# Performance work log

Measured on AMD Instinct MI355X. Metric: run time of the kernel, lower is better.

The kernel has to match this reference:

```python
import math
import jax, jax.numpy as jnp
import numpy as np
from jax import lax

HEADS = 8
DIM_HEAD = 32
DIM = 256
FF_INNER = DIM * 4
EPS = 1e-5


def conv1x1(x, w, b=None):
    # x: (B,C,H,W), w: (O,C)
    y = jnp.einsum('bchw,oc->bohw', x, w)
    return y if b is None else y + b[None, :, None, None]


def dwconv3(x, w, b):
    # depthwise 3x3, padding=1; w: (C,1,3,3)
    C = x.shape[1]
    y = lax.conv_general_dilated(x, w, (1, 1), 'SAME',
                                 dimension_numbers=('NCHW', 'OIHW', 'NCHW'),
                                 feature_group_count=C)
    return y + b[None, :, None, None]


def instance_norm(x):
    m = jnp.mean(x, axis=(2, 3), keepdims=True)
    v = jnp.var(x, axis=(2, 3), keepdims=True)
    return (x - m) / jnp.sqrt(v + EPS)


def chan_layer_norm(x, g, b):
    m = jnp.mean(x, axis=1, keepdims=True)
    v = jnp.var(x, axis=1, keepdims=True)
    return (x - m) / jnp.sqrt(v + EPS) * g + b


def l2norm(t):
    # F.normalize(t, dim=-1): normalize along last (width) axis
    n = jnp.sqrt(jnp.sum(t * t, axis=-1, keepdims=True))
    return t / jnp.maximum(n, 1e-12)


def dpsa(x, g, bc, w_qkv, w_out, b_out):
    B, C, H, W = x.shape
    kH = int(math.ceil(math.sqrt(H)))
    kW = int(math.ceil(math.sqrt(W)))
    x = chan_layer_norm(x, g, bc)
    qkv = conv1x1(x, w_qkv)                       # (B, 3*inner, H, W)
    q, k, v = jnp.split(qkv, 3, axis=1)
    fold = lambda t: t.reshape(B * HEADS, DIM_HEAD, H, W)
    q, k, v = fold(q), fold(k), fold(v)
    q, k = l2norm(q), l2norm(k)
    BH = B * HEADS
    q_probe = jnp.sum(jnp.abs(q), axis=(2, 3))    # (BH, d)
    if kH < H:
        k_height = jnp.sum(jnp.abs(k), axis=3)    # (BH, d, H)
        score_r = jnp.einsum('bc,bch->bh', q_probe, k_height)
        _, idx_h = lax.top_k(score_r, kH)          # (BH, kH)
        idx = jnp.broadcast_to(idx_h[:, None, :, None], (BH, DIM_HEAD, kH, W))
        k = jnp.take_along_axis(k, idx, axis=2)
        v = jnp.take_along_axis(v, idx, axis=2)
    if kW < W:
        k_width = jnp.sum(jnp.abs(k), axis=2)     # (BH, d, W)
        score_c = jnp.einsum('bc,bcw->bw', q_probe, k_width)
        _, idx_w = lax.top_k(score_c, kW)          # (BH, kW)
        idx = jnp.broadcast_to(idx_w[:, None, None, :], (BH, DIM_HEAD, k.shape[2], kW))
        k = jnp.take_along_axis(k, idx, axis=3)
        v = jnp.take_along_axis(v, idx, axis=3)
    flat = lambda t: t.transpose(0, 2, 3, 1).reshape(BH, -1, DIM_HEAD)
    q, k, v = flat(q), flat(k), flat(v)            # (BH, HW, d), (BH, kHkW, d)
    sim = jnp.einsum('bid,bjd->bij', q, k)         # note: original never applies scale
    attn = jax.nn.softmax(sim, axis=-1)
    out = jnp.einsum('bij,bjd->bid', attn, v)
    out = out.reshape(B, HEADS, H, W, DIM_HEAD).transpose(0, 1, 4, 2, 3)
    out = out.reshape(B, HEADS * DIM_HEAD, H, W)
    return conv1x1(out, w_out, b_out)


def hpb_forward(x, g, bc, w_qkv, w_out, b_out, w_dw, b_dw, w_comb, b_comb,
                w_ff1, b_ff1, w_ffdw, b_ffdw, w_ff2, b_ff2):
    attn_branch = dpsa(x, g, bc, w_qkv, w_out, b_out)
    conv_branch = dwconv3(x, w_dw, b_dw)
    combined = jnp.concatenate([attn_branch, conv_branch], axis=1)
    attn_out = conv1x1(combined, w_comb, b_comb) + x
    # feed-forward: 1x1 conv -> IN -> GELU -> Residual(dw3x3 -> IN -> GELU) -> 1x1 conv -> IN
    h = jax.nn.gelu(instance_norm(conv1x1(attn_out, w_ff1, b_ff1)), approximate=False)
    h = h + jax.nn.gelu(instance_norm(dwconv3(h, w_ffdw, b_ffdw)), approximate=False)
    return instance_norm(conv1x1(h, w_ff2, b_ff2))


def setup_inputs() -> dict:
    key = jax.random.key(0)
    ks = jax.random.split(key, 12)
    s = 0.02
    inner = HEADS * DIM_HEAD
    return {
        'x': jax.random.normal(ks[0], (16, DIM, 64, 64), dtype=jnp.float32),
        'g': jnp.ones((1, DIM, 1, 1), jnp.float32),
        'bc': jnp.zeros((1, DIM, 1, 1), jnp.float32),
        'w_qkv': jax.random.normal(ks[1], (inner * 3, DIM), jnp.float32) * s,
        'w_out': jax.random.normal(ks[2], (DIM, inner), jnp.float32) * s,
        'b_out': jnp.zeros((DIM,), jnp.float32),
        'w_dw': jax.random.normal(ks[3], (DIM, 1, 3, 3), jnp.float32) * s,
        'b_dw': jnp.zeros((DIM,), jnp.float32),
        'w_comb': jax.random.normal(ks[4], (DIM, DIM * 2), jnp.float32) * s,
        'b_comb': jnp.zeros((DIM,), jnp.float32),
        'w_ff1': jax.random.normal(ks[5], (FF_INNER, DIM), jnp.float32) * s,
        'b_ff1': jnp.zeros((FF_INNER,), jnp.float32),
        'w_ffdw': jax.random.normal(ks[6], (FF_INNER, 1, 3, 3), jnp.float32) * s,
        'b_ffdw': jnp.zeros((FF_INNER,), jnp.float32),
        'w_ff2': jax.random.normal(ks[7], (DIM, FF_INNER), jnp.float32) * s,
        'b_ff2': jnp.zeros((DIM,), jnp.float32),
    }


def reference(x, g, bc, w_qkv, w_out, b_out, w_dw, b_dw, w_comb, b_comb,
              w_ff1, b_ff1, w_ffdw, b_ffdw, w_ff2, b_ff2):
    return hpb_forward(x, g, bc, w_qkv, w_out, b_out, w_dw, b_dw, w_comb, b_comb,
                       w_ff1, b_ff1, w_ffdw, b_ffdw, w_ff2, b_ff2)
```

## Files before the change

### kernel.cpp

```cpp
#include <hip/hip_runtime.h>
#include <math.h>

#define NB 16
#define NC 256
#define NP 4096
#define NHEADS 8
#define NDH 32
#define NBH 128
#define NFF 1024
#define CEPS 1e-5f

typedef short s16x8 __attribute__((ext_vector_type(8)));
typedef float f32x4 __attribute__((ext_vector_type(4)));

__global__ __launch_bounds__(256) void diag_fill(float* __restrict__ out, float val, int n)
{
    int i = blockIdx.x * 256 + threadIdx.x;
    if (i < n) out[i] = val;
}

__device__ inline unsigned short f2bf(float f) {
    unsigned u = __float_as_uint(f);
    return (unsigned short)((u + 0x7FFFu + ((u >> 16) & 1u)) >> 16);
}
__device__ inline float bf2f(unsigned short h) { return __uint_as_float(((unsigned)h) << 16); }
__device__ inline void split2(float f, unsigned short& hi, unsigned short& lo) {
    hi = f2bf(f);
    lo = f2bf(f - bf2f(hi));
}
__device__ inline void split_rn(float f, unsigned short& hi, unsigned short& lo) {
    unsigned u = __float_as_uint(f);
    unsigned tt = u + 0x8000u;
    hi = (unsigned short)(tt >> 16);
    float r = f - __uint_as_float(tt & 0xffff0000u);
    lo = (unsigned short)((__float_as_uint(r) + 0x8000u) >> 16);
}
__device__ inline unsigned pack_hl(float f) {
    unsigned short h, lo; split2(f, h, lo);
    return ((unsigned)h << 16) | (unsigned)lo;
}
__device__ inline float packf(float f) { return __uint_as_float(pack_hl(f)); }

__global__ __launch_bounds__(256) void pack_wg_kernel(
    const float* __restrict__ w, const float* __restrict__ g,
    unsigned* __restrict__ pw, int n)
{
    int i = blockIdx.x * 256 + threadIdx.x;
    if (i < n) pw[i] = pack_hl(w[i] * g[i & 255]);
}

__global__ __launch_bounds__(256) void cln_stats_kernel(
    const float* __restrict__ x, float* __restrict__ rs, float* __restrict__ mrs)
{
    __shared__ double red[512];
    int t = threadIdx.x;
    int i = t & 63, q = t >> 6;
    int col = blockIdx.x * 64 + i;
    int b = col >> 12, p = col & 4095;
    const float* src = x + (size_t)b * NC * NP + (size_t)(q * 64) * NP + p;
    double s = 0.0, s2 = 0.0;
    #pragma unroll 8
    for (int c = 0; c < 64; c++) { float v = src[(size_t)c * NP]; s += v; s2 += (double)v * v; }
    red[q * 64 + i] = s; red[256 + q * 64 + i] = s2;
    __syncthreads();
    if (q == 0) {
        double S  = red[i] + red[64 + i] + red[128 + i] + red[192 + i];
        double S2 = red[256 + i] + red[320 + i] + red[384 + i] + red[448 + i];
        double mean = S * (1.0 / 256.0);
        double var = S2 * (1.0 / 256.0) - mean * mean;
        double r = 1.0 / sqrt(var + (double)CEPS);
        rs[col]  = (float)r;
        mrs[col] = (float)(mean * r);
    }
}

__global__ __launch_bounds__(256) void ab_kernel(
    const float* __restrict__ wq, const float* __restrict__ g, const float* __restrict__ bc,
    float* __restrict__ Aab, float* __restrict__ Bab)
{
    int o = blockIdx.x * 256 + threadIdx.x;
    if (o >= 768) return;
    double a = 0.0, bsum = 0.0;
    for (int c = 0; c < 256; c++) {
        double w = wq[o * 256 + c];
        a += w * (double)g[c];
        bsum += w * (double)bc[c];
    }
    Aab[o] = (float)a; Bab[o] = (float)bsum;
}

__global__ __launch_bounds__(256) void fuse_comb_kernel(
    const float* __restrict__ w_comb, const float* __restrict__ w_out,
    const float* __restrict__ b_out, const float* __restrict__ b_comb,
    unsigned* __restrict__ pwF, float* __restrict__ bF)
{
    int idx = blockIdx.x * 256 + threadIdx.x;
    int o = idx >> 9, cc = idx & 511;
    float val;
    if (cc < 256) {
        double s = 0.0;
        for (int k = 0; k < 256; k++)
            s += (double)w_comb[o * 512 + k] * (double)w_out[k * 256 + cc];
        val = (float)s;
    } else {
        val = w_comb[o * 512 + cc];
    }
    pwF[idx] = pack_hl(val);
    if (idx < 256) {
        double s = 0.0;
        for (int k = 0; k < 256; k++)
            s += (double)w_comb[idx * 512 + k] * (double)b_out[k];
        bF[idx] = (float)(s + (double)b_comb[idx]);
    }
}

template<bool PACKO, bool PACKA, bool CLN, bool OBF16, bool BBF16>
__global__ __launch_bounds__(512) void gemm_mfma(
    const float* __restrict__ inA, int sA, int C1,
    const float* __restrict__ inB, int sB, int Ctot,
    const float* __restrict__ Wt, const float* __restrict__ bias,
    const float* __restrict__ resid, float* __restrict__ out, int sO, int O,
    const float* __restrict__ rs, const float* __restrict__ mrs,
    const float* __restrict__ Aab, const float* __restrict__ Bab,
    float* __restrict__ qrow, float* __restrict__ kheight)
{
    __shared__ __align__(16) unsigned short Ah[128 * 32], Al[128 * 32];
    __shared__ __align__(16) unsigned short Bh[128 * 32];
    __shared__ __align__(16) unsigned short Bl[BBF16 ? 16 : 128 * 32];
    char* cAh = (char*)Ah; char* cAl = (char*)Al;
    char* cBh = (char*)Bh; char* cBl = (char*)Bl;

    const unsigned npb = gridDim.x * gridDim.y;
    unsigned lin = blockIdx.x + gridDim.x * (blockIdx.y + gridDim.y * blockIdx.z);
    unsigned low = lin & 7u, rest = lin >> 3;
    unsigned high = (rest >= npb) ? 1u : 0u;
    unsigned idx = rest - high * npb;
    const int b = (int)(low + 8u * high);
    const int o0 = (int)(idx / gridDim.x) * 128, p0 = (int)(idx % gridDim.x) * 128;

    const int t = threadIdx.x;
    const int l = t & 63, w = t >> 6;
    const int wr = w & 3, wc = w >> 2;
    const int g = l >> 4, l15 = l & 15;
    const int slotl = (l & 3) ^ ((l >> 2) & 3);

    f32x4 acc[2][4];
    #pragma unroll
    for (int m = 0; m < 2; m++)
        #pragma unroll
        for (int n = 0; n < 4; n++) acc[m][n] = (f32x4){0.f, 0.f, 0.f, 0.f};

    const int arow = t >> 2;
    const int ak8 = (t & 3) * 8;
    const int aslot = (arow & 3) ^ ((arow >> 2) & 3);
    const int aoff = arow * 64 + ((((ak8 >> 3)) ^ aslot) << 4);
    const int bp = t & 127;
    const int bhk = t >> 7;
    const int bslot = (bp & 3) ^ ((bp >> 2) & 3);
    const int boffst = bp * 64 + ((bhk ^ bslot) << 4);

    uint4 wa0, wa1;
    unsigned pb[8];

    #define LOAD_TILE(K0)                                                                 \
    {                                                                                     \
        const unsigned* wsrc = (const unsigned*)Wt + (size_t)(o0 + arow) * Ctot + (K0) + ak8; \
        wa0 = *(const uint4*)(wsrc);                                                      \
        wa1 = *(const uint4*)(wsrc + 4);                                                  \
        _Pragma("unroll")                                                                 \
        for (int q = 0; q < 4; q++) {                                                     \
            int c2 = bhk * 8 + q * 2;                                                     \
            int cc = (K0) + c2;                                                           \
            if constexpr (BBF16) {                                                        \
                const unsigned short* s16 = (cc < C1)                                     \
                    ? (const unsigned short*)inA + ((size_t)b * sA + cc) * (size_t)NP + p0 + bp \
                    : (const unsigned short*)inB + ((size_t)b * sB + (cc - C1)) * (size_t)NP + p0 + bp; \
                unsigned short v0 = s16[0];                                               \
                unsigned short v1 = s16[NP];                                              \
                pb[q] = (unsigned)v0 | ((unsigned)v1 << 16);                              \
            } else {                                                                      \
                const float* srcp = (cc < C1) ? inA + ((size_t)b * sA + cc) * (size_t)NP  \
                                              : inB + ((size_t)b * sB + (cc - C1)) * (size_t)NP; \
                pb[2 * q]     = __float_as_uint(srcp[p0 + bp]);                           \
                pb[2 * q + 1] = __float_as_uint(srcp[(size_t)NP + p0 + bp]);              \
            }                                                                             \
        }                                                                                 \
    }

    #define STORE_LDS()                                                                   \
    {                                                                                     \
        if constexpr (PACKA) {                                                            \
            uint4 hq, lq;                                                                 \
            hq.x = __builtin_amdgcn_perm(wa0.y, wa0.x, 0x07060302u);                      \
            lq.x = __builtin_amdgcn_perm(wa0.y, wa0.x, 0x05040100u);                      \
            hq.y = __builtin_amdgcn_perm(wa0.w, wa0.z, 0x07060302u);                      \
            lq.y = __builtin_amdgcn_perm(wa0.w, wa0.z, 0x05040100u);                      \
            hq.z = __builtin_amdgcn_perm(wa1.y, wa1.x, 0x07060302u);                      \
            lq.z = __builtin_amdgcn_perm(wa1.y, wa1.x, 0x05040100u);                      \
            hq.w = __builtin_amdgcn_perm(wa1.w, wa1.z, 0x07060302u);                      \
            lq.w = __builtin_amdgcn_perm(wa1.w, wa1.z, 0x05040100u);                      \
            *(uint4*)(cAh + aoff) = hq;                                                   \
            *(uint4*)(cAl + aoff) = lq;                                                   \
        } else {                                                                          \
            ushort4 h0, l0, h1, l1;                                                       \
            split_rn(__uint_as_float(wa0.x), h0.x, l0.x);                                 \
            split_rn(__uint_as_float(wa0.y), h0.y, l0.y);                                 \
            split_rn(__uint_as_float(wa0.z), h0.z, l0.z);                                 \
            split_rn(__uint_as_float(wa0.w), h0.w, l0.w);                                 \
            split_rn(__uint_as_float(wa1.x), h1.x, l1.x);                                 \
            split_rn(__uint_as_float(wa1.y), h1.y, l1.y);                                 \
            split_rn(__uint_as_float(wa1.z), h1.z, l1.z);                                 \
            split_rn(__uint_as_float(wa1.w), h1.w, l1.w);                                 \
            *(ushort4*)(cAh + aoff) = h0; *(ushort4*)(cAh + aoff + 8) = h1;               \
            *(ushort4*)(cAl + aoff) = l0; *(ushort4*)(cAl + aoff + 8) = l1;               \
        }                                                                                 \
        if constexpr (BBF16) {                                                            \
            *(uint4*)(cBh + boffst) = (uint4){pb[0], pb[1], pb[2], pb[3]};                \
        } else {                                                                          \
            unsigned hp[4], lp[4];                                                        \
            _Pragma("unroll")                                                             \
            for (int q = 0; q < 4; q++) {                                                 \
                unsigned u0 = pb[2 * q], u1 = pb[2 * q + 1];                              \
                if constexpr (CLN) {                                                      \
                    unsigned short sh0, sl0, sh1, sl1;                                    \
                    split_rn(__uint_as_float(u0), sh0, sl0);                              \
                    split_rn(__uint_as_float(u1), sh1, sl1);                              \
                    hp[q] = (unsigned)sh0 | ((unsigned)sh1 << 16);                        \
                    lp[q] = (unsigned)sl0 | ((unsigned)sl1 << 16);                        \
                } else {                                                                  \
                    hp[q] = __builtin_amdgcn_perm(u1, u0, 0x07060302u);                   \
                    lp[q] = __builtin_amdgcn_perm(u1, u0, 0x05040100u);                   \
                }                                                                         \
            }                                                                             \
            *(uint4*)(cBh + boffst) = (uint4){hp[0], hp[1], hp[2], hp[3]};                \
            *(uint4*)(cBl + boffst) = (uint4){lp[0], lp[1], lp[2], lp[3]};                \
        }                                                                                 \
    }

    LOAD_TILE(0)

    for (int k0 = 0; k0 < Ctot; k0 += 32) {
        if (k0) __syncthreads();
        STORE_LDS()
        __syncthreads();
        if (k0 + 32 < Ctot) LOAD_TILE(k0 + 32)

        s16x8 ah[2], al[2];
        #pragma unroll
        for (int m = 0; m < 2; m++) {
            int ao = (wr * 32 + m * 16 + l15) * 64 + ((g ^ slotl) << 4);
            ah[m] = *(const s16x8*)(cAh + ao);
            al[m] = *(const s16x8*)(cAl + ao);
        }
        #pragma unroll
        for (int n = 0; n < 4; n++) {
            int bo = (wc * 64 + n * 16 + l15) * 64 + ((g ^ slotl) << 4);
            s16x8 bh = *(const s16x8*)(cBh + bo);
            if constexpr (BBF16) {
                #pragma unroll
                for (int m = 0; m < 2; m++) {
                    acc[m][n] = __builtin_amdgcn_mfma_f32_16x16x32_bf16(ah[m], bh, acc[m][n], 0, 0, 0);
                    acc[m][n] = __builtin_amdgcn_mfma_f32_16x16x32_bf16(al[m], bh, acc[m][n], 0, 0, 0);
                }
            } else {
                s16x8 bl = *(const s16x8*)(cBl + bo);
                #pragma unroll
                for (int m = 0; m < 2; m++) {
                    acc[m][n] = __builtin_amdgcn_mfma_f32_16x16x32_bf16(ah[m], bh, acc[m][n], 0, 0, 0);
                    acc[m][n] = __builtin_amdgcn_mfma_f32_16x16x32_bf16(ah[m], bl, acc[m][n], 0, 0, 0);
                    acc[m][n] = __builtin_amdgcn_mfma_f32_16x16x32_bf16(al[m], bh, acc[m][n], 0, 0, 0);
                }
            }
        }
    }
    #undef LOAD_TILE
    #undef STORE_LDS

    #pragma unroll
    for (int m = 0; m < 2; m++) {
        #pragma unroll
        for (int r = 0; r < 4; r++) {
            int orow = o0 + wr * 32 + m * 16 + g * 4 + r;
            float bs = (!CLN && bias) ? bias[orow] : 0.f;
            float Ao = CLN ? Aab[orow] : 0.f;
            float Bo = CLN ? Bab[orow] : 0.f;
            if constexpr (CLN) {
                float vv[4];
                #pragma unroll
                for (int n = 0; n < 4; n++) {
                    int pcol = p0 + wc * 64 + n * 16 + l15;
                    size_t cidx = (size_t)b * NP + pcol;
                    vv[n] = rs[cidx] * acc[m][n][r] - mrs[cidx] * Ao + Bo;
                }
                int which = orow >> 8;
                if (which < 2) {
                    float ss = vv[0] * vv[0] + vv[1] * vv[1] + vv[2] * vv[2] + vv[3] * vv[3];
                    ss += __shfl_xor(ss, 1); ss += __shfl_xor(ss, 2);
                    ss += __shfl_xor(ss, 4); ss += __shfl_xor(ss, 8);
                    float inv = 1.f / fmaxf(sqrtf(ss), 1e-12f);
                    float as = 0.f;
                    #pragma unroll
                    for (int n = 0; n < 4; n++) { vv[n] *= inv; as += fabsf(vv[n]); }
                    as += __shfl_xor(as, 1); as += __shfl_xor(as, 2);
                    as += __shfl_xor(as, 4); as += __shfl_xor(as, 8);
                    if (l15 == 0) {
                        int idx2 = orow & 255;
                        int head = idx2 >> 5, c = idx2 & 31;
                        int h = (p0 >> 6) + wc;
                        int rr = ((b << 3) + head) * 2048 + c * 64 + h;
                        (which == 0 ? qrow : kheight)[rr] = as;
                    }
                }
                #pragma unroll
                for (int n = 0; n < 4; n++) {
                    int pcol = p0 + wc * 64 + n * 16 + l15;
                    out[((size_t)b * sO + orow) * (size_t)NP + pcol] = vv[n];
                }
            } else {
                #pragma unroll
                for (int n = 0; n < 4; n++) {
                    int pcol = p0 + wc * 64 + n * 16 + l15;
                    float v = acc[m][n][r] + bs;
                    if (resid) v += resid[((size_t)b * O + orow) * (size_t)NP + pcol];
                    size_t oidx = ((size_t)b * sO + orow) * (size_t)NP + pcol;
                    if constexpr (OBF16)
                        ((unsigned short*)out)[oidx] = f2bf(v);
                    else
                        out[oidx] = PACKO ? packf(v) : v;
                }
            }
        }
    }
}

__global__ __launch_bounds__(64) void select_kernel(
    const float* __restrict__ qkv, const float* __restrict__ qrow,
    const float* __restrict__ kheight,
    float* __restrict__ ksel, float* __restrict__ vsel)
{
    const int bh = blockIdx.x;
    const int b = bh >> 3, head = bh & 7;
    const int lane = threadIdx.x;
    __shared__ int hs[8], wsl[8];
    __shared__ float qp[32];
    if (lane < 32) {
        double s = 0.0;
        const float* qr = qrow + (size_t)bh * 2048 + lane * 64;
        for (int h = 0; h < 64; h++) s += qr[h];
        qp[lane] = (float)s;
    }
    __syncthreads();
    double scd = 0.0;
    for (int c = 0; c < 32; c++) scd += (double)qp[c] * kheight[((size_t)bh * 32 + c) * 64 + lane];
    float sc = (float)scd;
    for (int it = 0; it < 8; it++) {
        float v = sc; int id = lane;
        for (int off = 32; off; off >>= 1) {
            float ov = __shfl_xor(v, off); int oi = __shfl_xor(id, off);
            if (ov > v || (ov == v && oi < id)) { v = ov; id = oi; }
        }
        if (lane == 0) hs[it] = id;
        if (lane == id) sc = -3.4e38f;
    }
    __syncthreads();
    const float* kbase = qkv + ((size_t)b * 768 + 256 + head * 32) * NP;
    double sc2d = 0.0;
    for (int c = 0; c < 32; c++) {
        float kw = 0.f;
        for (int hi = 0; hi < 8; hi++)
            kw += fabsf(kbase[(size_t)c * NP + hs[hi] * 64 + lane]);
        sc2d += (double)qp[c] * kw;
    }
    float sc2 = (float)sc2d;
    for (int it = 0; it < 8; it++) {
        float v = sc2; int id = lane;
        for (int off = 32; off; off >>= 1) {
            float ov = __shfl_xor(v, off); int oi = __shfl_xor(id, off);
            if (ov > v || (ov == v && oi < id)) { v = ov; id = oi; }
        }
        if (lane == 0) wsl[it] = id;
        if (lane == id) sc2 = -3.4e38f;
    }
    __syncthreads();
    const float* vbase = qkv + ((size_t)b * 768 + 512 + head * 32) * NP;
    int hi = lane >> 3, wi = lane & 7;
    int hh = hs[hi], ww = wsl[wi];
    for (int d = 0; d < 32; d++) {
        ksel[((size_t)bh * 64 + lane) * 32 + d] = kbase[(size_t)d * NP + hh * 64 + ww];
        vsel[((size_t)bh * 64 + lane) * 32 + d] = vbase[(size_t)d * NP + hh * 64 + ww];
    }
}

__global__ __launch_bounds__(256) void attn_kernel(
    const float* __restrict__ qkv, const float* __restrict__ ksel, const float* __restrict__ vsel,
    unsigned short* __restrict__ ctxu)
{
    __shared__ __align__(16) float ks[64][32];
    __shared__ __align__(16) float vs[64][32];
    int bh = blockIdx.y, b = bh >> 3, head = bh & 7;
    int t = threadIdx.x;
    const float* kb = ksel + (size_t)bh * 2048;
    const float* vb = vsel + (size_t)bh * 2048;
    for (int i = 0; i < 8; i++) {
        ((float*)ks)[t + i * 256] = kb[t + i * 256];
        ((float*)vs)[t + i * 256] = vb[t + i * 256];
    }
    __syncthreads();
    int p = blockIdx.x * 256 + t;
    const float* qb = qkv + ((size_t)b * 768 + head * 32) * NP + p;
    unsigned short* ob = ctxu + ((size_t)b * 256 + head * 32) * NP + p;
    float q[32];
    #pragma unroll
    for (int d = 0; d < 32; d++) q[d] = qb[(size_t)d * NP];
    float s[64], m = -3.4e38f;
    for (int j = 0; j < 64; j++) {
        float dot = 0.f;
        #pragma unroll
        for (int d = 0; d < 32; d++) dot += q[d] * ks[j][d];
        s[j] = dot; m = fmaxf(m, dot);
    }
    float den = 0.f;
    for (int j = 0; j < 64; j++) { float e = expf(s[j] - m); s[j] = e; den += e; }
    float o[32] = {};
    for (int j = 0; j < 64; j++) {
        float a = s[j];
        #pragma unroll
        for (int d = 0; d < 32; d++) o[d] += a * vs[j][d];
    }
    float r = 1.f / den;
    #pragma unroll
    for (int d = 0; d < 32; d++) ob[(size_t)d * NP] = f2bf(o[d] * r);
}

__global__ __launch_bounds__(256) void dwconv_kernel(
    const float* __restrict__ in, const float* __restrict__ w, const float* __restrict__ bias,
    unsigned short* __restrict__ out, int Cn)
{
    __shared__ __align__(16) float pl[66][67];
    int bcb = blockIdx.x;
    int c = bcb % Cn;
    const float2* src2 = (const float2*)(in + (size_t)bcb * NP);
    unsigned* dst2 = (unsigned*)(out + (size_t)bcb * NP);
    int t = threadIdx.x;
    if (t < 66) { pl[0][t] = 0.f; pl[65][t] = 0.f; }
    if (t >= 66 && t < 130) { int rr = t - 65; pl[rr][0] = 0.f; pl[rr][65] = 0.f; }
    float w9[9];
    #pragma unroll
    for (int k = 0; k < 9; k++) w9[k] = w[c * 9 + k];
    float bsv = bias[c];
    #pragma unroll
    for (int i = 0; i < 8; i++) {
        float2 f = src2[i * 256 + t];
        int pix = i * 512 + 2 * t;
        int y = pix >> 6, xx = pix & 63;
        pl[y + 1][xx + 1] = f.x;
        pl[y + 1][xx + 2] = f.y;
    }
    __syncthreads();
    float vv[16];
    #pragma unroll
    for (int j = 0; j < 16; j++) {
        int pix = (j >> 1) * 512 + 2 * t + (j & 1);
        int y = pix >> 6, xx = pix & 63;
        float acc = bsv;
        #pragma unroll
        for (int dy = 0; dy < 3; dy++)
            #pragma unroll
            for (int dx = 0; dx < 3; dx++)
                acc += w9[dy * 3 + dx] * pl[y + dy][xx + dx];
        vv[j] = acc;
    }
    #pragma unroll
    for (int i = 0; i < 8; i++) {
        unsigned u = (unsigned)f2bf(vv[2 * i]) | ((unsigned)f2bf(vv[2 * i + 1]) << 16);
        dst2[i * 256 + t] = u;
    }
}

__device__ inline float gelu_fast(float x) {
    float z = x * 0.70710678118654752f;
    float a = fabsf(z);
    float t = 1.0f / (1.0f + 0.3275911f * a);
    float p = t * (0.254829592f + t * (-0.284496736f + t * (1.421413741f +
              t * (-1.453152027f + t * 1.061405429f))));
    float e = __expf(-a * a);
    float r = 1.0f - p * e;
    float erfz = copysignf(r, z);
    return 0.5f * x * (1.0f + erfz);
}

__device__ inline void block_reduceP(float a, float b, double* red, int t,
                                     double& A, double& B)
{
    __syncthreads();
    red[t] = (double)a; red[256 + t] = (double)b;
    __syncthreads();
    for (int st = 128; st; st >>= 1) {
        if (t < st) { red[t] += red[t + st]; red[256 + t] += red[256 + t + st]; }
        __syncthreads();
    }
    A = red[0]; B = red[256];
}

__device__ inline double block_reduce1(float s, double* red, int t)
{
    __syncthreads();
    red[t] = (double)s;
    __syncthreads();
    for (int st = 128; st; st >>= 1) {
        if (t < st) red[t] += red[t + st];
        __syncthreads();
    }
    return red[0];
}

__global__ __launch_bounds__(256) void ff_fused_kernel(
    unsigned short* __restrict__ h, const float* __restrict__ w, const float* __restrict__ bias)
{
    __shared__ __align__(16) float pl[66][67];
    __shared__ double red[512];
    int plane = blockIdx.x;
    int c = plane & (NFF - 1);
    const unsigned* h2 = (const unsigned*)(h + (size_t)plane * NP);
    unsigned* h2w = (unsigned*)(h + (size_t)plane * NP);
    int t = threadIdx.x;
    if (t < 66) { pl[0][t] = 0.f; pl[65][t] = 0.f; }
    if (t >= 66 && t < 130) { int rr = t - 65; pl[rr][0] = 0.f; pl[rr][65] = 0.f; }

    float v[16]; float sf = 0.f, s2f = 0.f;
    #pragma unroll
    for (int i = 0; i < 8; i++) {
        unsigned u = h2[i * 256 + t];
        float x0 = bf2f((unsigned short)(u & 0xffffu));
        float x1 = bf2f((unsigned short)(u >> 16));
        v[2 * i] = x0; v[2 * i + 1] = x1;
        sf += x0 + x1;
        s2f += x0 * x0 + x1 * x1;
    }
    double S, S2;
    block_reduceP(sf, s2f, red, t, S, S2);
    double mean = S * (1.0 / NP);
    double var = S2 * (1.0 / NP) - mean * mean;
    float rs = (float)(1.0 / sqrt(var + (double)CEPS));
    float mf = (float)mean;

    float w9[9];
    #pragma unroll
    for (int k = 0; k < 9; k++) w9[k] = w[c * 9 + k];
    float bsv = bias[c];

    #pragma unroll
    for (int j = 0; j < 16; j++) {
        int pix = (j >> 1) * 512 + 2 * t + (j & 1);
        float gx = gelu_fast((v[j] - mf) * rs);
        v[j] = gx;
        pl[(pix >> 6) + 1][(pix & 63) + 1] = gx;
    }
    __syncthreads();

    float tv[16]; float sg = 0.f, s2g = 0.f;
    #pragma unroll
    for (int j = 0; j < 16; j++) {
        int pix = (j >> 1) * 512 + 2 * t + (j & 1);
        int y = pix >> 6, xx = pix & 63;
        float acc = bsv;
        #pragma unroll
        for (int dy = 0; dy < 3; dy++)
            #pragma unroll
            for (int dx = 0; dx < 3; dx++)
                acc += w9[dy * 3 + dx] * pl[y + dy][xx + dx];
        tv[j] = acc; sg += acc; s2g += acc * acc;
    }
    double Sb, S2b;
    block_reduceP(sg, s2g, red, t, Sb, S2b);
    double mean2 = Sb * (1.0 / NP);
    double var2 = S2b * (1.0 / NP) - mean2 * mean2;
    float rs2 = (float)(1.0 / sqrt(var2 + (double)CEPS));
    float mf2 = (float)mean2;

    #pragma unroll
    for (int i = 0; i < 8; i++) {
        float o0 = v[2 * i]     + gelu_fast((tv[2 * i] - mf2) * rs2);
        float o1 = v[2 * i + 1] + gelu_fast((tv[2 * i + 1] - mf2) * rs2);
        unsigned u = (unsigned)f2bf(o0) | ((unsigned)f2bf(o1) << 16);
        h2w[i * 256 + t] = u;
    }
}

__global__ __launch_bounds__(256) void in_final_kernel(float* __restrict__ y)
{
    __shared__ double red[256];
    size_t base = (size_t)blockIdx.x * NP;
    int t = threadIdx.x;
    float v[16]; float sf = 0.f;
    #pragma unroll
    for (int i = 0; i < 16; i++) { float x = y[base + t + i * 256]; v[i] = x; sf += x; }
    double S = block_reduce1(sf, red, t);
    float mf = (float)(S * (1.0 / NP));
    float s2f = 0.f;
    #pragma unroll
    for (int i = 0; i < 16; i++) { float d = v[i] - mf; v[i] = d; s2f += d * d; }
    double S2 = block_reduce1(s2f, red, t);
    float rs = (float)(1.0 / sqrt(S2 * (1.0 / NP) + (double)CEPS));
    #pragma unroll
    for (int i = 0; i < 16; i++)
        y[base + t + i * 256] = v[i] * rs;
}

extern "C" void kernel_launch(void* const* d_in, const int* in_sizes, int n_in,
                              void* d_out, int out_size, void* d_ws, size_t ws_size,
                              hipStream_t stream)
{
    const float* x      = (const float*)d_in[0];
    const float* g      = (const float*)d_in[1];
    const float* bc     = (const float*)d_in[2];
    const float* w_qkv  = (const float*)d_in[3];
    const float* w_out  = (const float*)d_in[4];
    const float* b_out  = (const float*)d_in[5];
    const float* w_dw   = (const float*)d_in[6];
    const float* b_dw   = (const float*)d_in[7];
    const float* w_comb = (const float*)d_in[8];
    const float* b_comb = (const float*)d_in[9];
    const float* w_ff1  = (const float*)d_in[10];
    const float* b_ff1  = (const float*)d_in[11];
    const float* w_ffdw = (const float*)d_in[12];
    const float* b_ffdw = (const float*)d_in[13];
    const float* w_ff2  = (const float*)d_in[14];
    const float* b_ff2  = (const float*)d_in[15];
    float* out = (float*)d_out;
    float* ws  = (float*)d_ws;

    const size_t S = (size_t)NB * NC * NP;
    float* qkv   = ws + S;
    unsigned short* h1u   = (unsigned short*)ws;
    unsigned short* ctxu  = (unsigned short*)(ws + 2097152);
    unsigned short* convu = (unsigned short*)(ws + S);
    unsigned short* Fbufu = (unsigned short*)out;
    float* qrow    = ws;
    float* kheight = qrow + 262144;
    float* kselb   = kheight + 262144;
    float* vselb   = kselb + 262144;
    float* rs_a    = ws + 1052672;
    float* mrs_a   = rs_a + 65536;
    float* Aab     = mrs_a + 65536;
    float* Bab     = Aab + 768;
    unsigned* pw_qkv = (unsigned*)out;
    unsigned* pwF    = (unsigned*)ws;
    float*    bF     = ws + 131072;

    size_t need = 4 * S * sizeof(float);
    if (ws_size < need) {
        float val = 1024.0f + (float)(ws_size >> 20);
        diag_fill<<<(out_size + 255) / 256, 256, 0, stream>>>(out, val, out_size);
        return;
    }

    pack_wg_kernel<<<768, 256, 0, stream>>>(w_qkv, g, pw_qkv, 768 * 256);
    cln_stats_kernel<<<1024, 256, 0, stream>>>(x, rs_a, mrs_a);
    ab_kernel<<<3, 256, 0, stream>>>(w_qkv, g, bc, Aab, Bab);
    gemm_mfma<false, true, true, false, false><<<dim3(32, 6, NB), 512, 0, stream>>>(
        x, 256, 256, nullptr, 0, 256, (const float*)pw_qkv, nullptr, nullptr, qkv, 768, 768,
        rs_a, mrs_a, Aab, Bab, qrow, kheight);
    select_kernel<<<NBH, 64, 0, stream>>>(qkv, qrow, kheight, kselb, vselb);
    attn_kernel<<<dim3(16, NBH), 256, 0, stream>>>(qkv, kselb, vselb, ctxu);
    fuse_comb_kernel<<<512, 256, 0, stream>>>(w_comb, w_out, b_out, b_comb, pwF, bF);
    dwconv_kernel<<<NB * NC, 256, 0, stream>>>(x, w_dw, b_dw, convu, NC);
    gemm_mfma<false, true, false, true, true><<<dim3(32, 2, NB), 512, 0, stream>>>(
        (const float*)ctxu, 256, 256, (const float*)convu, 256, 512,
        (const float*)pwF, bF, x, (float*)Fbufu, 256, 256,
        nullptr, nullptr, nullptr, nullptr, nullptr, nullptr);
    gemm_mfma<false, false, false, true, true><<<dim3(32, 8, NB), 512, 0, stream>>>(
        (const float*)Fbufu, 256, 256, nullptr, 0, 256, w_ff1, b_ff1, nullptr, (float*)h1u,
        1024, 1024, nullptr, nullptr, nullptr, nullptr, nullptr, nullptr);
    ff_fused_kernel<<<NB * NFF, 256, 0, stream>>>(h1u, w_ffdw, b_ffdw);
    gemm_mfma<false, false, false, false, true><<<dim3(32, 2, NB), 512, 0, stream>>>(
        (const float*)h1u, 1024, 1024, nullptr, 0, 1024, w_ff2, b_ff2, nullptr, out, 256, 256,
        nullptr, nullptr, nullptr, nullptr, nullptr, nullptr);
    in_final_kernel<<<NB * NC, 256, 0, stream>>>(out);
}
```

Before: 779.0 us.

## Compute V only at selected top-k positions instead of full V projection

```diff
diff --git a/kernel.cpp b/kernel.cpp
--- a/kernel.cpp
+++ b/kernel.cpp
@@ -336,7 +336,7 @@
 __global__ __launch_bounds__(64) void select_kernel(
     const float* __restrict__ qkv, const float* __restrict__ qrow,
     const float* __restrict__ kheight,
-    float* __restrict__ ksel, float* __restrict__ vsel)
+    float* __restrict__ ksel, int* __restrict__ hswsl)
 {
     const int bh = blockIdx.x;
     const int b = bh >> 3, head = bh & 7;
@@ -382,12 +382,57 @@
         if (lane == id) sc2 = -3.4e38f;
     }
     __syncthreads();
-    const float* vbase = qkv + ((size_t)b * 768 + 512 + head * 32) * NP;
+    if (lane < 8) hswsl[bh * 16 + lane] = hs[lane];
+    else if (lane < 16) hswsl[bh * 16 + lane] = wsl[lane - 8];
     int hi = lane >> 3, wi = lane & 7;
     int hh = hs[hi], ww = wsl[wi];
-    for (int d = 0; d < 32; d++) {
+    for (int d = 0; d < 32; d++)
         ksel[((size_t)bh * 64 + lane) * 32 + d] = kbase[(size_t)d * NP + hh * 64 + ww];
-        vsel[((size_t)bh * 64 + lane) * 32 + d] = vbase[(size_t)d * NP + hh * 64 + ww];
+}
+
+__global__ __launch_bounds__(256) void vsel_kernel(
+    const float* __restrict__ x, const float* __restrict__ w_qkv, const float* __restrict__ g,
+    const int* __restrict__ hswsl, const float* __restrict__ rs, const float* __restrict__ mrs,
+    const float* __restrict__ Aab, const float* __restrict__ Bab,
+    float* __restrict__ vsel)
+{
+    __shared__ float Wg[32][257];
+    __shared__ float xcol[16][257];
+    __shared__ int pos_s[16];
+    const int bh = blockIdx.y, b = bh >> 3, head = bh & 7;
+    const int t = threadIdx.x;
+    for (int i = t; i < 8192; i += 256) {
+        int d = i >> 8, c = i & 255;
+        Wg[d][c] = w_qkv[(size_t)(512 + head * 32 + d) * 256 + c] * g[c];
+    }
+    if (t < 16) {
+        int j = blockIdx.x * 16 + t;
+        int hh = hswsl[bh * 16 + (j >> 3)];
+        int ww = hswsl[bh * 16 + 8 + (j & 7)];
+        pos_s[t] = hh * 64 + ww;
+    }
+    __syncthreads();
+    for (int i = t; i < 4096; i += 256) {
+        int jj = i >> 8, c = i & 255;
+        xcol[jj][c] = x[((size_t)b * 256 + c) * (size_t)NP + pos_s[jj]];
+    }
+    __syncthreads();
+    const int l = t & 63, w = t >> 6;
+    const int d = l & 31, ch = l >> 5;
+    const float Av = Aab[512 + head * 32 + d];
+    const float Bv = Bab[512 + head * 32 + d];
+    for (int q = 0; q < 4; q++) {
+        int jj = w * 4 + q;
+        float s = 0.f;
+        #pragma unroll
+        for (int c = 0; c < 128; c++) s += Wg[d][ch * 128 + c] * xcol[jj][ch * 128 + c];
+        s += __shfl_xor(s, 32);
+        if (ch == 0) {
+            int j = blockIdx.x * 16 + jj;
+            size_t cidx = (size_t)b * NP + pos_s[jj];
+            float val = rs[cidx] * s - mrs[cidx] * Av + Bv;
+            vsel[((size_t)bh * 64 + j) * 32 + d] = val;
+        }
     }
 }
 
@@ -640,6 +685,7 @@
     float* kheight = qrow + 262144;
     float* kselb   = kheight + 262144;
     float* vselb   = kselb + 262144;
+    int*   hswsl   = (int*)(ws + 1048576);
     float* rs_a    = ws + 1052672;
     float* mrs_a   = rs_a + 65536;
     float* Aab     = mrs_a + 65536;
@@ -655,13 +701,15 @@
         return;
     }
 
-    pack_wg_kernel<<<768, 256, 0, stream>>>(w_qkv, g, pw_qkv, 768 * 256);
+    pack_wg_kernel<<<512, 256, 0, stream>>>(w_qkv, g, pw_qkv, 512 * 256);
     cln_stats_kernel<<<1024, 256, 0, stream>>>(x, rs_a, mrs_a);
     ab_kernel<<<3, 256, 0, stream>>>(w_qkv, g, bc, Aab, Bab);
-    gemm_mfma<false, true, true, false, false><<<dim3(32, 6, NB), 512, 0, stream>>>(
-        x, 256, 256, nullptr, 0, 256, (const float*)pw_qkv, nullptr, nullptr, qkv, 768, 768,
+    gemm_mfma<false, true, true, false, false><<<dim3(32, 4, NB), 512, 0, stream>>>(
+        x, 256, 256, nullptr, 0, 256, (const float*)pw_qkv, nullptr, nullptr, qkv, 768, 512,
         rs_a, mrs_a, Aab, Bab, qrow, kheight);
-    select_kernel<<<NBH, 64, 0, stream>>>(qkv, qrow, kheight, kselb, vselb);
+    select_kernel<<<NBH, 64, 0, stream>>>(qkv, qrow, kheight, kselb, hswsl);
+    vsel_kernel<<<dim3(4, NBH), 256, 0, stream>>>(x, w_qkv, g, hswsl, rs_a, mrs_a,
+                                                  Aab, Bab, vselb);
     attn_kernel<<<dim3(16, NBH), 256, 0, stream>>>(qkv, kselb, vselb, ctxu);
     fuse_comb_kernel<<<512, 256, 0, stream>>>(w_comb, w_out, b_out, b_comb, pwF, bF);
     dwconv_kernel<<<NB * NC, 256, 0, stream>>>(x, w_dw, b_dw, convu, NC);
```

Result: no change. 772.6 us (-0.8%).
